# Optimization experiments

Measured on AMD Instinct MI355X. Metric: run time of the kernel, lower is better.

The kernel has to match this reference:

```python
import jax, jax.numpy as jnp
import numpy as np

N = 8192      # num nodes
E = 131072    # num edges (avg degree 16)
B = 2         # batch
F_NODE = 128
F_EDGE = 64
H = 256       # hidden_dim
L = 3         # num_layers


def setup_inputs() -> dict:
    key = jax.random.key(0)
    ks = jax.random.split(key, 16)
    # unique edges, sorted row-major to match the original i-then-j loop order
    rng = np.random.default_rng(0)
    lin = np.sort(rng.choice(N * N, size=E, replace=False))
    src = jnp.asarray(lin // N, dtype=jnp.int32)
    dst = jnp.asarray(lin % N, dtype=jnp.int32)
    adjacency = jnp.zeros((N, N), jnp.float32).at[src, dst].set(1.0)

    s = 0.05
    return {
        "node_features": jax.random.normal(ks[0], (B, N, F_NODE), jnp.float32),
        "edge_features": jax.random.normal(ks[1], (B, E, F_EDGE), jnp.float32),
        "adjacency": adjacency,
        "src_idx": src,
        "dst_idx": dst,
        "W_ne": jax.random.normal(ks[2], (F_NODE, H), jnp.float32) * s,
        "b_ne": jnp.zeros((H,), jnp.float32),
        "W_ee": jax.random.normal(ks[3], (F_EDGE, H), jnp.float32) * s,
        "b_ee": jnp.zeros((H,), jnp.float32),
        "W_conv": jax.random.normal(ks[4], (L, H, H), jnp.float32) * s,
        "b_conv": jnp.zeros((L, H), jnp.float32),
        "W_cls": jax.random.normal(ks[5], (H, 5), jnp.float32) * s,
        "b_cls": jnp.zeros((5,), jnp.float32),
        "W_ep": jax.random.normal(ks[6], (2 * H, 1), jnp.float32) * s,
        "b_ep": jnp.zeros((1,), jnp.float32),
        "W_gp": jax.random.normal(ks[7], (H, 1), jnp.float32) * s,
        "b_gp": jnp.zeros((1,), jnp.float32),
    }


def reference(node_features, edge_features, adjacency, src_idx, dst_idx,
              W_ne, b_ne, W_ee, b_ee, W_conv, b_conv,
              W_cls, b_cls, W_ep, b_ep, W_gp, b_gp):
    # embeddings (eval mode: dropout is identity)
    h = jax.nn.relu(node_features @ W_ne + b_ne)          # [B,N,H]
    e = jax.nn.relu(edge_features @ W_ee + b_ee)          # [B,E,H] (computed, unused downstream as in original)
    # message-passing layers: messages = A @ h, then linear+relu+residual
    for l in range(L):
        m = jnp.einsum('ij,bjh->bih', adjacency, h)       # dense adjacency matmul
        o = jax.nn.relu(m @ W_conv[l] + b_conv[l])
        h = o + h                                          # residual (in==out dim)
    node_health = h @ W_cls + b_cls                        # [B,N,5]
    # fused edge prediction over all nonzero adjacency entries (row-major order)
    h_src = h[:, src_idx, :]                               # [B,E,H]
    h_dst = h[:, dst_idx, :]                               # [B,E,H]
    edge_repr = jnp.concatenate([h_src, h_dst], axis=-1)   # [B,E,2H]
    edge_propagation = jax.nn.sigmoid(edge_repr @ W_ep + b_ep)  # [B,E,1]
    global_repr = jnp.mean(h, axis=1)                      # [B,H]
    system_health = jax.nn.sigmoid(global_repr @ W_gp + b_gp)   # [B,1]
    return (node_health, edge_propagation, system_health, h)
```

## Files before the change

### kernel.cpp

```cpp
#include <hip/hip_runtime.h>
#include <hip/hip_bf16.h>

typedef __bf16 bf16_t;
typedef __bf16 bf16x8 __attribute__((ext_vector_type(8)));
typedef float f32x4 __attribute__((ext_vector_type(4)));

#define N_NODES 8192
#define N_EDGES 131072
#define HDIM    256


__device__ inline int rowblk_swz(int x) {
  int xcd = x & 7, q = x >> 3;
  return (xcd >> 2) * 128 + (xcd & 3) * 32 + q;
}

__device__ inline float wred(float v) {
#pragma unroll
  for (int m = 32; m; m >>= 1) v += __shfl_xor(v, m);
  return v;
}

__global__ __launch_bounds__(256) void gemm1_prep_k(const float* __restrict__ nf,
                                                    const float* __restrict__ Wne,
                                                    const float* __restrict__ bne,
                                                    const float* __restrict__ Wconv,
                                                    const int* __restrict__ src,
                                                    int* __restrict__ rp,
                                                    bf16_t* __restrict__ WconvT,
                                                    bf16_t* __restrict__ hs0) {
  int x = blockIdx.x, tid = threadIdx.x;
  if (x >= 1024) {
    if (x < 1057) {
      int i = (x - 1024) * 256 + tid;
      if (i < N_NODES) {
        int lo = 0, hi = N_EDGES;
        while (lo < hi) { int mid = (lo + hi) >> 1; if (src[mid] < i) lo = mid + 1; else hi = mid; }
        rp[i] = lo;
      } else if (i == N_NODES) {
        rp[i] = N_EDGES;
      }
    } else {
      int u = (x - 1057) * 256 + tid;
      int l = u / 65536, r = u % 65536;
      int n = r / 256, k = r % 256;
      WconvT[l * 65536 + n * 256 + k] = (bf16_t)Wconv[l * 65536 + k * 256 + n];
    }
    return;
  }
  __shared__ bf16_t Wlds[64 * 128];
  int xb = x & 255, yb = x >> 8;
  int cg0 = yb * 64;
  for (int k = tid >> 6; k < 128; k += 4) {
    int lc = tid & 63;
    float w = Wne[k * 256 + cg0 + lc];
    Wlds[lc * 128 + (((k >> 3) ^ (lc & 15)) << 3) + (k & 7)] = (bf16_t)w;
  }
  int lane = tid & 63, wv = tid >> 6;
  int r0 = (rowblk_swz(xb) * 4 + wv) * 16;
  int l15 = lane & 15, l4 = lane >> 4;
  bf16x8 a[4];
  const float* Ap = nf + (size_t)(r0 + l15) * 128 + 8 * l4;
#pragma unroll
  for (int kk = 0; kk < 4; ++kk) {
    f32x4 a0 = *(const f32x4*)(Ap + 32 * kk);
    f32x4 a1 = *(const f32x4*)(Ap + 32 * kk + 4);
#pragma unroll
    for (int j = 0; j < 4; ++j) { a[kk][j] = (bf16_t)a0[j]; a[kk][4 + j] = (bf16_t)a1[j]; }
  }
  __syncthreads();
#pragma unroll
  for (int ct = 0; ct < 4; ++ct) {
    int lc0 = ct * 16;
    f32x4 acc = {0.f, 0.f, 0.f, 0.f};
#pragma unroll
    for (int kk = 0; kk < 4; ++kk) {
      bf16x8 b = *(const bf16x8*)&Wlds[(lc0 + l15) * 128 + (((4 * kk + l4) ^ l15) << 3)];
      acc = __builtin_amdgcn_mfma_f32_16x16x32_bf16(a[kk], b, acc, 0, 0, 0);
    }
    int col = cg0 + lc0 + l15;
    float bv = bne[col];
#pragma unroll
    for (int i = 0; i < 4; ++i) {
      int row = r0 + 4 * l4 + i;
      size_t idx = (size_t)row * HDIM + col;
      hs0[idx] = (bf16_t)fmaxf(acc[i] + bv, 0.f);
    }
  }
}

__global__ __launch_bounds__(256) void gconv_k(const bf16_t* __restrict__ hs_in,
                                               const int* __restrict__ rp,
                                               const int* __restrict__ dst,
                                               const bf16_t* __restrict__ BT,
                                               const float* __restrict__ bias,
                                               bf16_t* __restrict__ hs_out) {
  __shared__ bf16_t A_lds[16 * 256];
  int tid = threadIdx.x;
  int x = blockIdx.x;
  int xcd = x & 7, q = x >> 3;
  int b = xcd >> 2;
  int blk = (xcd & 3) * 128 + q;
  int i0 = blk * 16;
  int gang = tid >> 5, l32 = tid & 31;
  const bf16_t* hb = hs_in + (size_t)b * (N_NODES * HDIM) + l32 * 8;
#pragma unroll
  for (int r2 = 0; r2 < 2; ++r2) {
    int lrow = gang * 2 + r2;
    int i = i0 + lrow;
    int e0 = rp[i], e1 = rp[i + 1];
    float acc[8] = {0.f, 0.f, 0.f, 0.f, 0.f, 0.f, 0.f, 0.f};
    int e = e0;
    for (; e + 8 <= e1; e += 8) {
      bf16x8 v[8];
#pragma unroll
      for (int u = 0; u < 8; ++u) v[u] = *(const bf16x8*)(hb + (size_t)dst[e + u] * HDIM);
#pragma unroll
      for (int u = 0; u < 8; ++u)
#pragma unroll
        for (int jj = 0; jj < 8; ++jj) acc[jj] += (float)v[u][jj];
    }
    for (; e < e1; ++e) {
      bf16x8 v = *(const bf16x8*)(hb + (size_t)dst[e] * HDIM);
#pragma unroll
      for (int jj = 0; jj < 8; ++jj) acc[jj] += (float)v[jj];
    }
    bf16x8 o;
#pragma unroll
    for (int jj = 0; jj < 8; ++jj) o[jj] = (bf16_t)acc[jj];
    *(bf16x8*)&A_lds[lrow * 256 + ((l32 ^ (lrow & 7)) * 8)] = o;
  }
  __syncthreads();
  int lane = tid & 63, wv = tid >> 6;
  int l15 = lane & 15, l4 = lane >> 4;
  bf16x8 a[8];
#pragma unroll
  for (int kk = 0; kk < 8; ++kk)
    a[kk] = *(const bf16x8*)&A_lds[l15 * 256 + (((kk * 4 + l4) ^ (l15 & 7)) * 8)];
  int row_base = b * N_NODES + i0;
#pragma unroll
  for (int ct = 0; ct < 4; ++ct) {
    int c0 = wv * 64 + ct * 16;
    const bf16_t* Bp = BT + (size_t)(c0 + l15) * HDIM + 8 * l4;
    f32x4 acc = {0.f, 0.f, 0.f, 0.f};
#pragma unroll
    for (int kk = 0; kk < 8; ++kk)
      acc = __builtin_amdgcn_mfma_f32_16x16x32_bf16(a[kk], *(const bf16x8*)(Bp + 32 * kk), acc, 0, 0, 0);
    int col = c0 + l15;
    float bv = bias[col];
#pragma unroll
    for (int ii = 0; ii < 4; ++ii) {
      int row = row_base + 4 * l4 + ii;
      size_t idx = (size_t)row * HDIM + col;
      float v = fmaxf(acc[ii] + bv, 0.f) + (float)hs_in[idx];
      hs_out[idx] = (bf16_t)v;
    }
  }
}

__global__ __launch_bounds__(256) void gconv_heads_k(const bf16_t* __restrict__ hs_in,
                                                     const int* __restrict__ rp,
                                                     const int* __restrict__ dst,
                                                     const bf16_t* __restrict__ BT,
                                                     const float* __restrict__ bias,
                                                     float* __restrict__ out_h,
                                                     const float* __restrict__ Wcls,
                                                     const float* __restrict__ bcls,
                                                     const float* __restrict__ Wep,
                                                     const float* __restrict__ Wgp,
                                                     float* __restrict__ ds,
                                                     float* __restrict__ dd,
                                                     float* __restrict__ pg,
                                                     float* __restrict__ out_nh) {
  __shared__ bf16_t A_lds[16 * 256];
  __shared__ float red[4][16][8];
  __shared__ float pgrow[16];
  int tid = threadIdx.x;
  int x = blockIdx.x;
  int xcd = x & 7, q = x >> 3;
  int b = xcd >> 2;
  int blk = (xcd & 3) * 128 + q;
  int i0 = blk * 16;
  int gang = tid >> 5, l32 = tid & 31;
  const bf16_t* hb = hs_in + (size_t)b * (N_NODES * HDIM) + l32 * 8;
#pragma unroll
  for (int r2 = 0; r2 < 2; ++r2) {
    int lrow = gang * 2 + r2;
    int i = i0 + lrow;
    int e0 = rp[i], e1 = rp[i + 1];
    float acc[8] = {0.f, 0.f, 0.f, 0.f, 0.f, 0.f, 0.f, 0.f};
    int e = e0;
    for (; e + 8 <= e1; e += 8) {
      bf16x8 v[8];
#pragma unroll
      for (int u = 0; u < 8; ++u) v[u] = *(const bf16x8*)(hb + (size_t)dst[e + u] * HDIM);
#pragma unroll
      for (int u = 0; u < 8; ++u)
#pragma unroll
        for (int jj = 0; jj < 8; ++jj) acc[jj] += (float)v[u][jj];
    }
    for (; e < e1; ++e) {
      bf16x8 v = *(const bf16x8*)(hb + (size_t)dst[e] * HDIM);
#pragma unroll
      for (int jj = 0; jj < 8; ++jj) acc[jj] += (float)v[jj];
    }
    bf16x8 o;
#pragma unroll
    for (int jj = 0; jj < 8; ++jj) o[jj] = (bf16_t)acc[jj];
    *(bf16x8*)&A_lds[lrow * 256 + ((l32 ^ (lrow & 7)) * 8)] = o;
  }
  __syncthreads();
  int lane = tid & 63, wv = tid >> 6;
  int l15 = lane & 15, l4 = lane >> 4;
  bf16x8 a[8];
#pragma unroll
  for (int kk = 0; kk < 8; ++kk)
    a[kk] = *(const bf16x8*)&A_lds[l15 * 256 + (((kk * 4 + l4) ^ (l15 & 7)) * 8)];
  int row_base = b * N_NODES + i0;
  float p[4][8];
#pragma unroll
  for (int ii = 0; ii < 4; ++ii)
#pragma unroll
    for (int hh = 0; hh < 8; ++hh) p[ii][hh] = 0.f;
#pragma unroll
  for (int ct = 0; ct < 4; ++ct) {
    int c0 = wv * 64 + ct * 16;
    const bf16_t* Bp = BT + (size_t)(c0 + l15) * HDIM + 8 * l4;
    f32x4 acc = {0.f, 0.f, 0.f, 0.f};
#pragma unroll
    for (int kk = 0; kk < 8; ++kk)
      acc = __builtin_amdgcn_mfma_f32_16x16x32_bf16(a[kk], *(const bf16x8*)(Bp + 32 * kk), acc, 0, 0, 0);
    int col = c0 + l15;
    float bv = bias[col];
    float wc0 = Wcls[col * 5 + 0], wc1 = Wcls[col * 5 + 1], wc2 = Wcls[col * 5 + 2];
    float wc3 = Wcls[col * 5 + 3], wc4 = Wcls[col * 5 + 4];
    float wes = Wep[col], wed = Wep[256 + col], wgv = Wgp[col];
#pragma unroll
    for (int ii = 0; ii < 4; ++ii) {
      int row = row_base + 4 * l4 + ii;
      size_t idx = (size_t)row * HDIM + col;
      float v = fmaxf(acc[ii] + bv, 0.f) + (float)hs_in[idx];
      out_h[idx] = v;
      p[ii][0] += v * wc0; p[ii][1] += v * wc1; p[ii][2] += v * wc2;
      p[ii][3] += v * wc3; p[ii][4] += v * wc4;
      p[ii][5] += v * wes; p[ii][6] += v * wed; p[ii][7] += v * wgv;
    }
  }
#pragma unroll
  for (int ii = 0; ii < 4; ++ii)
#pragma unroll
    for (int hh = 0; hh < 8; ++hh) {
      float v = p[ii][hh];
#pragma unroll
      for (int m = 8; m; m >>= 1) v += __shfl_xor(v, m);
      p[ii][hh] = v;
    }
  if (l15 == 0) {
#pragma unroll
    for (int ii = 0; ii < 4; ++ii)
#pragma unroll
      for (int hh = 0; hh < 8; ++hh) red[wv][4 * l4 + ii][hh] = p[ii][hh];
  }
  __syncthreads();
  if (tid < 128) {
    int rl = tid >> 3, hh = tid & 7;
    float s = red[0][rl][hh] + red[1][rl][hh] + red[2][rl][hh] + red[3][rl][hh];
    int grow = row_base + rl;
    if (hh < 5)      out_nh[(size_t)grow * 5 + hh] = s + bcls[hh];
    else if (hh == 5) ds[grow] = s;
    else if (hh == 6) dd[grow] = s;
    else              pgrow[rl] = s;
  }
  __syncthreads();
  if (tid == 0) {
    float t = 0.f;
#pragma unroll
    for (int rl = 0; rl < 16; ++rl) t += pgrow[rl];
    pg[b * 512 + blk] = t;
  }
}

__global__ __launch_bounds__(256) void edge_sys_k(const float* __restrict__ ds,
                                                  const float* __restrict__ dd,
                                                  const int* __restrict__ src,
                                                  const int* __restrict__ dst,
                                                  const float* __restrict__ bep,
                                                  const float* __restrict__ pg,
                                                  const float* __restrict__ bgp,
                                                  float* __restrict__ out_ep,
                                                  float* __restrict__ out_sys) {
  int x = blockIdx.x;
  if (x < 1024) {
    int t = x * 256 + threadIdx.x;
    int b = t >> 17;
    int e = t & (N_EDGES - 1);
    float v = ds[(b << 13) + src[e]] + dd[(b << 13) + dst[e]] + bep[0];
    out_ep[t] = 1.f / (1.f + expf(-v));
  } else {
    int b = x - 1024, t = threadIdx.x;
    float v = pg[b * 512 + t] + pg[b * 512 + 256 + t];
    v = wred(v);
    __shared__ float sm[4];
    if ((t & 63) == 0) sm[t >> 6] = v;
    __syncthreads();
    if (t == 0) {
      float tot = sm[0] + sm[1] + sm[2] + sm[3];
      float g = tot / (float)N_NODES + bgp[0];
      out_sys[b] = 1.f / (1.f + expf(-g));
    }
  }
}

extern "C" void kernel_launch(void* const* d_in, const int* in_sizes, int n_in,
                              void* d_out, int out_size, void* d_ws, size_t ws_size,
                              hipStream_t stream) {
  (void)in_sizes; (void)n_in; (void)out_size; (void)ws_size;
  const float* nf    = (const float*)d_in[0];
  const int*   src   = (const int*)d_in[3];
  const int*   dst   = (const int*)d_in[4];
  const float* Wne   = (const float*)d_in[5];
  const float* bne   = (const float*)d_in[6];
  const float* Wconv = (const float*)d_in[9];
  const float* bconv = (const float*)d_in[10];
  const float* Wcls  = (const float*)d_in[11];
  const float* bcls  = (const float*)d_in[12];
  const float* Wep   = (const float*)d_in[13];
  const float* bep   = (const float*)d_in[14];
  const float* Wgp   = (const float*)d_in[15];
  const float* bgp   = (const float*)d_in[16];

  char* ws = (char*)d_ws;
  bf16_t* hs0    = (bf16_t*)(ws + 0);
  bf16_t* hs1    = (bf16_t*)(ws + 8388608);
  bf16_t* WconvT = (bf16_t*)(ws + 16777216);
  int*    rp     = (int*)(ws + 17170432);
  float*  ds     = (float*)(ws + 17207296);
  float*  dd     = (float*)(ws + 17272832);
  float*  pg     = (float*)(ws + 17338368);

  float* out     = (float*)d_out;
  float* out_nh  = out;
  float* out_ep  = out + 81920;
  float* out_sys = out + 344064;
  float* out_h   = out + 344066;

  hipLaunchKernelGGL(gemm1_prep_k, dim3(1825), dim3(256), 0, stream,
                     nf, Wne, bne, Wconv, src, rp, WconvT, hs0);
  hipLaunchKernelGGL(gconv_k, dim3(1024), dim3(256), 0, stream,
                     hs0, rp, dst, WconvT, bconv, hs1);
  hipLaunchKernelGGL(gconv_k, dim3(1024), dim3(256), 0, stream,
                     hs1, rp, dst, WconvT + 65536, bconv + 256, hs0);
  hipLaunchKernelGGL(gconv_heads_k, dim3(1024), dim3(256), 0, stream,
                     hs0, rp, dst, WconvT + 131072, bconv + 512, out_h,
                     Wcls, bcls, Wep, Wgp, ds, dd, pg, out_nh);
  hipLaunchKernelGGL(edge_sys_k, dim3(1026), dim3(256), 0, stream, ds, dd, src, dst, bep,
                     pg, bgp, out_ep, out_sys);
}
```

Before: 131.5 us.

## Double graph-conv row tile to 32 with 512-thread blocks; tile Wconv transpose

The graph-conv kernels now handle 32 node rows per block with 8 waves instead of 16 rows with 4 waves. Waves are split into a 2x4 row-by-column grid, so each Wconv column slice loaded from global is reused across twice as many rows. Partial reductions and the system-health sum are resized to match. The Wconv fp32-to-bf16 transpose also changes from an uncoalesced per-element scatter to a 64x64 shared-memory tiled transpose with padding, which cuts its block count. In exchange, larger blocks and fewer of them (512) may lower occupancy and load balance across the 256 CUs.

```diff
diff --git a/kernel.cpp b/kernel.cpp
--- a/kernel.cpp
+++ b/kernel.cpp
@@ -29,6 +29,7 @@
                                                     int* __restrict__ rp,
                                                     bf16_t* __restrict__ WconvT,
                                                     bf16_t* __restrict__ hs0) {
+  __shared__ char smem[64 * 65 * 4];
   int x = blockIdx.x, tid = threadIdx.x;
   if (x >= 1024) {
     if (x < 1057) {
@@ -41,14 +42,26 @@
         rp[i] = N_EDGES;
       }
     } else {
-      int u = (x - 1057) * 256 + tid;
-      int l = u / 65536, r = u % 65536;
-      int n = r / 256, k = r % 256;
-      WconvT[l * 65536 + n * 256 + k] = (bf16_t)Wconv[l * 65536 + k * 256 + n];
+      float (*tl)[65] = (float(*)[65])smem;
+      int t = x - 1057;
+      int l = t >> 4, tile = t & 15;
+      int tr = (tile >> 2) * 64, tc = (tile & 3) * 64;
+      int j = tid & 63, i0 = tid >> 6;
+#pragma unroll
+      for (int s = 0; s < 16; ++s) {
+        int i = 4 * s + i0;
+        tl[i][j] = Wconv[l * 65536 + (tr + i) * 256 + tc + j];
+      }
+      __syncthreads();
+#pragma unroll
+      for (int s = 0; s < 16; ++s) {
+        int i = 4 * s + i0;
+        WconvT[l * 65536 + (tc + i) * 256 + tr + j] = (bf16_t)tl[j][i];
+      }
     }
     return;
   }
-  __shared__ bf16_t Wlds[64 * 128];
+  bf16_t* Wlds = (bf16_t*)smem;
   int xb = x & 255, yb = x >> 8;
   int cg0 = yb * 64;
   for (int k = tid >> 6; k < 128; k += 4) {
@@ -89,19 +102,19 @@
   }
 }
 
-__global__ __launch_bounds__(256) void gconv_k(const bf16_t* __restrict__ hs_in,
+__global__ __launch_bounds__(512) void gconv_k(const bf16_t* __restrict__ hs_in,
                                                const int* __restrict__ rp,
                                                const int* __restrict__ dst,
                                                const bf16_t* __restrict__ BT,
                                                const float* __restrict__ bias,
                                                bf16_t* __restrict__ hs_out) {
-  __shared__ bf16_t A_lds[16 * 256];
+  __shared__ bf16_t A_lds[32 * 256];
   int tid = threadIdx.x;
   int x = blockIdx.x;
   int xcd = x & 7, q = x >> 3;
   int b = xcd >> 2;
-  int blk = (xcd & 3) * 128 + q;
-  int i0 = blk * 16;
+  int blk = (xcd & 3) * 64 + q;
+  int i0 = blk * 32;
   int gang = tid >> 5, l32 = tid & 31;
   const bf16_t* hb = hs_in + (size_t)b * (N_NODES * HDIM) + l32 * 8;
 #pragma unroll
@@ -132,15 +145,16 @@
   }
   __syncthreads();
   int lane = tid & 63, wv = tid >> 6;
+  int wr = wv >> 2, wc = wv & 3;
   int l15 = lane & 15, l4 = lane >> 4;
   bf16x8 a[8];
 #pragma unroll
   for (int kk = 0; kk < 8; ++kk)
-    a[kk] = *(const bf16x8*)&A_lds[l15 * 256 + (((kk * 4 + l4) ^ (l15 & 7)) * 8)];
-  int row_base = b * N_NODES + i0;
+    a[kk] = *(const bf16x8*)&A_lds[(wr * 16 + l15) * 256 + (((kk * 4 + l4) ^ (l15 & 7)) * 8)];
+  int row_base = b * N_NODES + i0 + wr * 16;
 #pragma unroll
   for (int ct = 0; ct < 4; ++ct) {
-    int c0 = wv * 64 + ct * 16;
+    int c0 = wc * 64 + ct * 16;
     const bf16_t* Bp = BT + (size_t)(c0 + l15) * HDIM + 8 * l4;
     f32x4 acc = {0.f, 0.f, 0.f, 0.f};
 #pragma unroll
@@ -158,7 +172,7 @@
   }
 }
 
-__global__ __launch_bounds__(256) void gconv_heads_k(const bf16_t* __restrict__ hs_in,
+__global__ __launch_bounds__(512) void gconv_heads_k(const bf16_t* __restrict__ hs_in,
                                                      const int* __restrict__ rp,
                                                      const int* __restrict__ dst,
                                                      const bf16_t* __restrict__ BT,
@@ -172,15 +186,15 @@
                                                      float* __restrict__ dd,
                                                      float* __restrict__ pg,
                                                      float* __restrict__ out_nh) {
-  __shared__ bf16_t A_lds[16 * 256];
-  __shared__ float red[4][16][8];
-  __shared__ float pgrow[16];
+  __shared__ bf16_t A_lds[32 * 256];
+  __shared__ float red[2][4][16][8];
+  __shared__ float pgrow[32];
   int tid = threadIdx.x;
   int x = blockIdx.x;
   int xcd = x & 7, q = x >> 3;
   int b = xcd >> 2;
-  int blk = (xcd & 3) * 128 + q;
-  int i0 = blk * 16;
+  int blk = (xcd & 3) * 64 + q;
+  int i0 = blk * 32;
   int gang = tid >> 5, l32 = tid & 31;
   const bf16_t* hb = hs_in + (size_t)b * (N_NODES * HDIM) + l32 * 8;
 #pragma unroll
@@ -211,12 +225,13 @@
   }
   __syncthreads();
   int lane = tid & 63, wv = tid >> 6;
+  int wr = wv >> 2, wc = wv & 3;
   int l15 = lane & 15, l4 = lane >> 4;
   bf16x8 a[8];
 #pragma unroll
   for (int kk = 0; kk < 8; ++kk)
-    a[kk] = *(const bf16x8*)&A_lds[l15 * 256 + (((kk * 4 + l4) ^ (l15 & 7)) * 8)];
-  int row_base = b * N_NODES + i0;
+    a[kk] = *(const bf16x8*)&A_lds[(wr * 16 + l15) * 256 + (((kk * 4 + l4) ^ (l15 & 7)) * 8)];
+  int row_base = b * N_NODES + i0 + wr * 16;
   float p[4][8];
 #pragma unroll
   for (int ii = 0; ii < 4; ++ii)
@@ -224,7 +239,7 @@
     for (int hh = 0; hh < 8; ++hh) p[ii][hh] = 0.f;
 #pragma unroll
   for (int ct = 0; ct < 4; ++ct) {
-    int c0 = wv * 64 + ct * 16;
+    int c0 = wc * 64 + ct * 16;
     const bf16_t* Bp = BT + (size_t)(c0 + l15) * HDIM + 8 * l4;
     f32x4 acc = {0.f, 0.f, 0.f, 0.f};
 #pragma unroll
@@ -259,13 +274,14 @@
 #pragma unroll
     for (int ii = 0; ii < 4; ++ii)
 #pragma unroll
-      for (int hh = 0; hh < 8; ++hh) red[wv][4 * l4 + ii][hh] = p[ii][hh];
-  }
-  __syncthreads();
-  if (tid < 128) {
+      for (int hh = 0; hh < 8; ++hh) red[wr][wc][4 * l4 + ii][hh] = p[ii][hh];
+  }
+  __syncthreads();
+  if (tid < 256) {
     int rl = tid >> 3, hh = tid & 7;
-    float s = red[0][rl][hh] + red[1][rl][hh] + red[2][rl][hh] + red[3][rl][hh];
-    int grow = row_base + rl;
+    float s = red[rl >> 4][0][rl & 15][hh] + red[rl >> 4][1][rl & 15][hh] +
+              red[rl >> 4][2][rl & 15][hh] + red[rl >> 4][3][rl & 15][hh];
+    int grow = b * N_NODES + i0 + rl;
     if (hh < 5)      out_nh[(size_t)grow * 5 + hh] = s + bcls[hh];
     else if (hh == 5) ds[grow] = s;
     else if (hh == 6) dd[grow] = s;
@@ -275,8 +291,8 @@
   if (tid == 0) {
     float t = 0.f;
 #pragma unroll
-    for (int rl = 0; rl < 16; ++rl) t += pgrow[rl];
-    pg[b * 512 + blk] = t;
+    for (int rl = 0; rl < 32; ++rl) t += pgrow[rl];
+    pg[b * 256 + blk] = t;
   }
 }
 
@@ -298,7 +314,7 @@
     out_ep[t] = 1.f / (1.f + expf(-v));
   } else {
     int b = x - 1024, t = threadIdx.x;
-    float v = pg[b * 512 + t] + pg[b * 512 + 256 + t];
+    float v = pg[b * 256 + t];
     v = wred(v);
     __shared__ float sm[4];
     if ((t & 63) == 0) sm[t >> 6] = v;
@@ -344,13 +360,13 @@
   float* out_sys = out + 344064;
   float* out_h   = out + 344066;
 
-  hipLaunchKernelGGL(gemm1_prep_k, dim3(1825), dim3(256), 0, stream,
+  hipLaunchKernelGGL(gemm1_prep_k, dim3(1105), dim3(256), 0, stream,
                      nf, Wne, bne, Wconv, src, rp, WconvT, hs0);
-  hipLaunchKernelGGL(gconv_k, dim3(1024), dim3(256), 0, stream,
+  hipLaunchKernelGGL(gconv_k, dim3(512), dim3(512), 0, stream,
                      hs0, rp, dst, WconvT, bconv, hs1);
-  hipLaunchKernelGGL(gconv_k, dim3(1024), dim3(256), 0, stream,
+  hipLaunchKernelGGL(gconv_k, dim3(512), dim3(512), 0, stream,
                      hs1, rp, dst, WconvT + 65536, bconv + 256, hs0);
-  hipLaunchKernelGGL(gconv_heads_k, dim3(1024), dim3(256), 0, stream,
+  hipLaunchKernelGGL(gconv_heads_k, dim3(512), dim3(512), 0, stream,
                      hs0, rp, dst, WconvT + 131072, bconv + 512, out_h,
                      Wcls, bcls, Wep, Wgp, ds, dd, pg, out_nh);
   hipLaunchKernelGGL(edge_sys_k, dim3(1026), dim3(256), 0, stream, ds, dd, src, dst, bep,
```

After: 114.0 us. 13.3% less time.
